# Optimization experiments

Hardware: AMD Instinct MI355X
Metric: run time of the kernel (lower is better)

The kernel has to match this reference:

```python
import jax, jax.numpy as jnp
import numpy as np

B, C, H, W = 8, 256, 64, 64
HEADS, HID = 8, 64
TMP = HEADS * HID  # 512


def setup_inputs() -> dict:
    key = jax.random.key(0)
    ks = jax.random.split(key, 6)
    s = lambda fan: 1.0 / np.sqrt(fan)
    fmap = jax.random.normal(ks[0], (B, C, H, W), jnp.float32)
    Wq = jax.random.normal(ks[1], (TMP, C), jnp.float32) * s(C)          # to_q 1x1 conv (no bias)
    Wdw = jax.random.normal(ks[2], (C, 1, 3, 3), jnp.float32) * s(9)     # depthwise 3x3 (groups=C, no bias)
    Wkv = jax.random.normal(ks[3], (2 * TMP, C), jnp.float32) * s(C)     # 1x1 conv producing k,v (no bias)
    Wout = jax.random.normal(ks[4], (C, TMP), jnp.float32) * s(TMP)      # to_out 1x1 conv
    bout = jax.random.normal(ks[5], (C,), jnp.float32) * 0.01
    return {"fmap": fmap, "Wq": Wq, "Wdw": Wdw, "Wkv": Wkv, "Wout": Wout, "bout": bout}


def reference(fmap, Wq, Wdw, Wkv, Wout, bout):
    heads, hid = HEADS, HID
    scale = hid ** (-0.5)
    b, c, h, w = fmap.shape
    n = h * w

    # 1x1 conv == channel GEMM
    q = jnp.einsum('bcxy,oc->boxy', fmap, Wq)
    # depthwise 3x3, padding=1
    dw = jax.lax.conv_general_dilated(
        fmap, Wdw, window_strides=(1, 1), padding='SAME',
        dimension_numbers=('NCHW', 'OIHW', 'NCHW'), feature_group_count=c)
    kv = jnp.einsum('bcxy,oc->boxy', dw, Wkv)
    k, v = jnp.split(kv, 2, axis=1)

    # 'b (h c) x y -> b h (x y) c'
    def to_seq(t):
        return t.reshape(b, heads, hid, n).transpose(0, 1, 3, 2)  # [b, h, n, d]

    q, k, v = to_seq(q), to_seq(k), to_seq(v)
    q = jax.nn.softmax(q, axis=-1) * scale   # softmax over feature dim
    k = jax.nn.softmax(k, axis=-2)           # softmax over token dim

    ctx = jnp.einsum('bhnd,bhne->bhde', k, v)    # [b, h, d, d]
    out = jnp.einsum('bhnd,bhde->bhne', q, ctx)  # [b, h, n, d]

    # '(b h) (x y) d -> b (h d) x y'
    out = out.transpose(0, 1, 3, 2).reshape(b, heads * hid, h, w)

    # to_out: GELU (exact) then 1x1 conv with bias (mode='ac')
    out = jax.nn.gelu(out, approximate=False)
    return jnp.einsum('bcxy,oc->boxy', out, Wout) + bout[None, :, None, None]
```

## Files before the change

kernel.cpp:

```cpp
#include <hip/hip_runtime.h>
#include <hip/hip_bf16.h>
#include <math.h>

#define Bx 8
#define Cc 256
#define Nn 4096
#define TMPc 512

typedef unsigned short ushort;
typedef unsigned int uint;
typedef unsigned long long ull;
typedef __attribute__((ext_vector_type(8))) short bf16x8;
typedef __attribute__((ext_vector_type(4))) float f32x4;

union F4 { float4 v; float f[4]; };

__device__ __forceinline__ ushort f2bf(float x) {
  uint u = __float_as_uint(x);
  uint r = (u + 0x7fffu + ((u >> 16) & 1u)) >> 16;
  return (ushort)r;
}
__device__ __forceinline__ float gelu_fast(float x) {
  float u = 0.70710678118654752f * x;
  float au = fabsf(u);
  float t = __builtin_amdgcn_rcpf(1.0f + 0.3275911f * au);
  float poly = ((((1.061405429f * t - 1.453152027f) * t + 1.421413741f) * t -
                 0.284496736f) * t + 0.254829592f) * t;
  float e = 1.0f - poly * __expf(-u * u);
  float erfu = copysignf(e, u);
  return 0.5f * x * (1.0f + erfu);
}

typedef const __attribute__((address_space(1))) uint* gp1_t;
typedef __attribute__((address_space(3))) uint* lp3_t;
__device__ __forceinline__ void gload16(void* lds, const void* g) {
  __builtin_amdgcn_global_load_lds((gp1_t)g, (lp3_t)lds, 16, 0, 0);
}
__device__ __forceinline__ void lgkm_fence() {
  asm volatile("s_waitcnt lgkmcnt(0)" ::: "memory");
}
__device__ __forceinline__ bf16x8 fragread(const char* lds, int row, int kc) {
  return *(const bf16x8*)(lds + row * 64 + ((kc ^ (row & 3)) << 4));
}
__device__ __forceinline__ void stage2(char* buf, const ushort* src, int ld,
                                       int row0, int col, int w, int prow, int gst) {
  int off = __builtin_amdgcn_readfirstlane(w * 2048);
  gload16(buf + off, src + (size_t)(row0 + prow) * ld + col + gst * 8);
  gload16(buf + off + 1024, src + (size_t)(row0 + 16 + prow) * ld + col + gst * 8);
}

#define CGRP 32
__global__ __launch_bounds__(256) void convfuse_k(const float* __restrict__ fmap,
                                                  const float* __restrict__ Wdw,
                                                  ushort* __restrict__ fmapT,
                                                  ushort* __restrict__ dwT) {
  __shared__ float sin_[CGRP][6 * 64 + 1];
  __shared__ float wl[CGRP][9];
  int t = threadIdx.x;
  int y0 = blockIdx.x * 4;
  int c0 = blockIdx.y * CGRP;
  int z = blockIdx.z;
  for (int i = t; i < CGRP * 9; i += 256) wl[i / 9][i % 9] = Wdw[c0 * 9 + i];
  const float* src = fmap + ((size_t)z * Cc + c0) * 4096;
#pragma unroll
  for (int it = 0; it < 12; ++it) {
    int idx = it * 256 + t;
    int c = idx / 96, rem = idx % 96, yy = rem >> 4, x4 = rem & 15;
    int gy = y0 - 1 + yy;
    F4 v;
    if ((unsigned)gy < 64u)
      v.v = *(const float4*)&src[(size_t)c * 4096 + gy * 64 + x4 * 4];
    else
      v.f[0] = v.f[1] = v.f[2] = v.f[3] = 0.f;
#pragma unroll
    for (int j = 0; j < 4; ++j) sin_[c][yy * 64 + x4 * 4 + j] = v.f[j];
  }
  __syncthreads();
  int c8 = (t & 3) * 8;
  int nl = t >> 2;
  size_t nbase = (size_t)z * 4096 + (size_t)y0 * 64;
#pragma unroll
  for (int it = 0; it < 4; ++it) {
    int n = it * 64 + nl;
    int y = n >> 6, x = n & 63;
    union { ushort u[8]; uint4 q; } fo, go;
#pragma unroll
    for (int cc = 0; cc < 8; ++cc) {
      int c = c8 + cc;
      fo.u[cc] = f2bf(sin_[c][(y + 1) * 64 + x]);
      float acc = 0.f;
#pragma unroll
      for (int dy = 0; dy < 3; ++dy) {
#pragma unroll
        for (int dx = 0; dx < 3; ++dx) {
          int xx = x + dx - 1;
          float pv = ((unsigned)xx < 64u) ? sin_[c][(y + dy) * 64 + xx] : 0.f;
          acc += pv * wl[c][dy * 3 + dx];
        }
      }
      go.u[cc] = f2bf(acc);
    }
    *(uint4*)&fmapT[(nbase + n) * Cc + c0 + c8] = fo.q;
    *(uint4*)&dwT[(nbase + n) * Cc + c0 + c8] = go.q;
  }
}

__global__ __launch_bounds__(256) void cvtb3_k(const float* __restrict__ Wq,
                                               const float* __restrict__ Wkv,
                                               const float* __restrict__ Wout,
                                               ushort* __restrict__ WqB,
                                               ushort* __restrict__ WkvB,
                                               ushort* __restrict__ WoutB) {
  int i = blockIdx.x * 256 + threadIdx.x;
  const float* s;
  ushort* d;
  int idx;
  if (i < 32768) { s = Wq; d = WqB; idx = i; }
  else if (i < 98304) { s = Wkv; d = WkvB; idx = i - 32768; }
  else { s = Wout; d = WoutB; idx = i - 98304; }
  F4 v; v.v = *(const float4*)&s[(size_t)idx * 4];
  union { ushort u[4]; uint2 q; } o;
#pragma unroll
  for (int j = 0; j < 4; ++j) o.u[j] = f2bf(v.f[j]);
  *(uint2*)&d[(size_t)idx * 4] = o.q;
}

__global__ __launch_bounds__(256, 2) void kvgemm3_k(const ushort* __restrict__ WkvB,
                                                    const ushort* __restrict__ dwT,
                                                    ushort* __restrict__ kv) {
  __shared__ __align__(16) char lds[57344];
  char* Bres = lds;
  char* Asg  = lds + 32768;
  int t = threadIdx.x, w = t >> 6, l = t & 63;
  int z = blockIdx.y, n0 = blockIdx.x * 64;
  int rl = l & 15, kc = l >> 4;
  int prow = l >> 2;
  int gst = (l & 3) ^ ((l >> 2) & 3);

  const ushort* dT = dwT + ((size_t)z * 4096 + n0) * 256;
#pragma unroll
  for (int p = 0; p < 8; ++p) {
    int row = (w * 8 + p) * 2 + (l >> 5);
    int cs = l & 31;
    int off = __builtin_amdgcn_readfirstlane((w * 8 + p) * 1024);
    gload16(Bres + off, dT + (size_t)row * 256 + ((cs ^ (row & 7)) * 8));
  }
  stage2(Asg, WkvB, 256, w * 32, 0, w, prow, gst);
  stage2(Asg + 8192, WkvB, 256, w * 32, 32, w, prow, gst);
  asm volatile("s_waitcnt vmcnt(0)" ::: "memory");
  __syncthreads();

  ushort* kz = kv + (size_t)z * 1024 * 4096;
#pragma unroll
  for (int c = 0; c < 8; ++c) {
    f32x4 acc[2][4];
#pragma unroll
    for (int i = 0; i < 2; ++i)
#pragma unroll
      for (int j = 0; j < 4; ++j) acc[i][j] = (f32x4){0.f, 0.f, 0.f, 0.f};
#pragma unroll
    for (int k0 = 0; k0 < 8; ++k0) {
      int s = c * 8 + k0;
      if (s + 2 < 64) {
        int s2 = s + 2;
        lgkm_fence();
        stage2(Asg + (s2 % 3) * 8192, WkvB, 256, (s2 >> 3) * 128 + w * 32,
               (s2 & 7) * 32, w, prow, gst);
      }
      if (s < 62) asm volatile("s_waitcnt vmcnt(4)" ::: "memory");
      else if (s == 62) asm volatile("s_waitcnt vmcnt(2)" ::: "memory");
      else asm volatile("s_waitcnt vmcnt(0)" ::: "memory");
      const char* bp = Asg + (s % 3) * 8192 + w * 2048;
      bf16x8 a0 = fragread(bp, rl, kc);
      bf16x8 a1 = fragread(bp, 16 + rl, kc);
#pragma unroll
      for (int j = 0; j < 4; ++j) {
        int n = 16 * j + rl;
        bf16x8 b = *(const bf16x8*)(Bres + n * 512 + (((k0 * 4 + kc) ^ (n & 7)) << 4));
        acc[0][j] = __builtin_amdgcn_mfma_f32_16x16x32_bf16(a0, b, acc[0][j], 0, 0, 0);
        acc[1][j] = __builtin_amdgcn_mfma_f32_16x16x32_bf16(a1, b, acc[1][j], 0, 0, 0);
      }
    }
#pragma unroll
    for (int i = 0; i < 2; ++i) {
#pragma unroll
      for (int reg = 0; reg < 4; ++reg) {
        int r = c * 128 + w * 32 + 16 * i + 4 * kc + reg;
#pragma unroll
        for (int j = 0; j < 4; ++j) {
          int col = n0 + 16 * j + rl;
          float v = acc[i][j][reg];
          kz[(size_t)r * 4096 + col] = f2bf(c < 4 ? __expf(v) : v);
        }
      }
    }
  }
}

__global__ __launch_bounds__(256) void ctx_mfma(const ushort* __restrict__ kv,
                                                float* __restrict__ ctxf,
                                                float* __restrict__ sf) {
  __shared__ __align__(16) char lds[16384];
  int t = threadIdx.x, w = t >> 6, l = t & 63;
  int s = blockIdx.x;
  int h = blockIdx.y & 7, z = blockIdx.y >> 3;
  const ushort* kb = kv + ((size_t)z * 1024 + h * 64) * 4096;
  const ushort* vb = kv + ((size_t)z * 1024 + 512 + h * 64) * 4096;
  f32x4 acc[2][2];
  f32x4 accs[2];
#pragma unroll
  for (int i = 0; i < 2; ++i) {
    accs[i] = (f32x4){0.f, 0.f, 0.f, 0.f};
#pragma unroll
    for (int j = 0; j < 2; ++j) acc[i][j] = (f32x4){0.f, 0.f, 0.f, 0.f};
  }
  bf16x8 ones;
#pragma unroll
  for (int i = 0; i < 8; ++i) ones[i] = (short)0x3F80;
  int wr = (w >> 1) * 32, wc = (w & 1) * 32;
  int rl = l & 15, kc = l >> 4;
  int srow = (l >> 2) & 15, scol = l & 3;
  int row = w * 16 + srow;
  int g = scol ^ (row & 3);
  int soff = __builtin_amdgcn_readfirstlane(w * 1024);
#define CSTG(bb, it)                                                      \
  {                                                                       \
    int k0_ = s * 512 + (it) * 32;                                        \
    gload16(lds + (bb) + soff, vb + (size_t)row * 4096 + k0_ + g * 8);    \
    gload16(lds + (bb) + 4096 + soff, kb + (size_t)row * 4096 + k0_ + g * 8); \
  }
  CSTG(0, 0);
  asm volatile("s_waitcnt vmcnt(0)" ::: "memory");
  __syncthreads();
  for (int it = 0; it < 16; ++it) {
    int cur = (it & 1) << 13;
    if (it + 1 < 16) CSTG(cur ^ 8192, it + 1);
    bf16x8 a[2], b[2];
#pragma unroll
    for (int i = 0; i < 2; ++i) a[i] = fragread(lds + cur, wr + i * 16 + rl, kc);
#pragma unroll
    for (int i = 0; i < 2; ++i) b[i] = fragread(lds + cur + 4096, wc + i * 16 + rl, kc);
#pragma unroll
    for (int i = 0; i < 2; ++i)
#pragma unroll
      for (int j = 0; j < 2; ++j)
        acc[i][j] = __builtin_amdgcn_mfma_f32_16x16x32_bf16(a[i], b[j], acc[i][j], 0, 0, 0);
    if (w < 2) {
#pragma unroll
      for (int j = 0; j < 2; ++j)
        accs[j] = __builtin_amdgcn_mfma_f32_16x16x32_bf16(b[j], ones, accs[j], 0, 0, 0);
    }
    asm volatile("s_waitcnt vmcnt(0)" ::: "memory");
    __syncthreads();
  }
  float* cf = ctxf + (size_t)(z * 8 + h) * 4096;
#pragma unroll
  for (int i = 0; i < 2; ++i)
#pragma unroll
    for (int reg = 0; reg < 4; ++reg) {
      int e = wr + i * 16 + kc * 4 + reg;
#pragma unroll
      for (int j = 0; j < 2; ++j) {
        int d = wc + j * 16 + rl;
        atomicAdd(&cf[e * 64 + d], acc[i][j][reg]);
      }
    }
  if (w < 2 && rl == 0) {
    float* sp = sf + (size_t)(z * 8 + h) * 64;
#pragma unroll
    for (int j = 0; j < 2; ++j)
#pragma unroll
      for (int reg = 0; reg < 4; ++reg)
        atomicAdd(&sp[wc + j * 16 + kc * 4 + reg], accs[j][reg]);
  }
#undef CSTG
}

__global__ __launch_bounds__(256) void ctx_cvt(const float* __restrict__ ctxf,
                                               const float* __restrict__ sf,
                                               ushort* __restrict__ ctxb) {
  int page = blockIdx.x;
  const float* s = ctxf + (size_t)page * 4096;
  const float* sp = sf + (size_t)page * 64;
  ushort* d = ctxb + (size_t)page * 4096;
  int t = threadIdx.x;
  int e = t >> 2, d0 = (t & 3) * 16;
  union { ushort u[16]; uint4 q[2]; } o;
#pragma unroll
  for (int j = 0; j < 16; ++j) {
    int dd = d0 + j;
    o.u[j] = f2bf(s[e * 64 + dd] / sp[dd]);
  }
  uint4* dp = (uint4*)&d[e * 64 + d0];
  dp[0] = o.q[0]; dp[1] = o.q[1];
}

__global__ __launch_bounds__(256, 2) void qao_k(const ushort* __restrict__ fmapT,
                                                const ushort* __restrict__ WqB,
                                                const ushort* __restrict__ ctxb,
                                                const ushort* __restrict__ WoutB,
                                                const float* __restrict__ bout,
                                                float* __restrict__ out) {
  __shared__ __align__(16) char lds[73728];
  __shared__ float wsum[4][64];
  char* qbuf = lds;
  char* Bres = lds + 16384;
  char* Asg  = lds + 49152;
  int t = threadIdx.x, w = t >> 6, l = t & 63;
  int z = blockIdx.y, n0 = blockIdx.x * 64;
  int rl = l & 15, kc = l >> 4;
  int prow = l >> 2;
  int gst = (l & 3) ^ ((l >> 2) & 3);
  int hh = w >> 1;
  int wcn = (w & 1) * 32;

  const ushort* fT = fmapT + ((size_t)z * 4096 + n0) * 256;
#pragma unroll
  for (int p = 0; p < 8; ++p) {
    int row = (w * 8 + p) * 2 + (l >> 5);
    int cs = l & 31;
    int off = __builtin_amdgcn_readfirstlane((w * 8 + p) * 1024);
    gload16(Bres + off, fT + (size_t)row * 256 + ((cs ^ (row & 7)) * 8));
  }
  stage2(Asg, WqB, 256, w * 32, 0, w, prow, gst);
  stage2(Asg + 8192, WqB, 256, w * 32, 32, w, prow, gst);

  f32x4 oacc[4][4];
#pragma unroll
  for (int i = 0; i < 4; ++i)
#pragma unroll
    for (int j = 0; j < 4; ++j) oacc[i][j] = (f32x4){0.f, 0.f, 0.f, 0.f};

  asm volatile("s_waitcnt vmcnt(0)" ::: "memory");
  __syncthreads();

  for (int c = 0; c < 4; ++c) {
    const ushort* Wqc = WqB + (size_t)(c * 128) * 256;
    f32x4 qa[2][4];
#pragma unroll
    for (int i = 0; i < 2; ++i)
#pragma unroll
      for (int j = 0; j < 4; ++j) qa[i][j] = (f32x4){0.f, 0.f, 0.f, 0.f};
#pragma unroll
    for (int k0 = 0; k0 < 8; ++k0) {
      if (k0 + 2 < 8) {
        lgkm_fence();
        stage2(Asg + ((k0 + 2) % 3) * 8192, Wqc, 256, w * 32, (k0 + 2) * 32, w, prow, gst);
      }
      if (k0 < 6) asm volatile("s_waitcnt vmcnt(4)" ::: "memory");
      else if (k0 == 6) asm volatile("s_waitcnt vmcnt(2)" ::: "memory");
      else asm volatile("s_waitcnt vmcnt(0)" ::: "memory");
      const char* bp = Asg + (k0 % 3) * 8192 + w * 2048;
      bf16x8 a0 = fragread(bp, rl, kc);
      bf16x8 a1 = fragread(bp, 16 + rl, kc);
#pragma unroll
      for (int j = 0; j < 4; ++j) {
        int n = 16 * j + rl;
        bf16x8 b = *(const bf16x8*)(Bres + n * 512 + (((k0 * 4 + kc) ^ (n & 7)) << 4));
        qa[0][j] = __builtin_amdgcn_mfma_f32_16x16x32_bf16(a0, b, qa[0][j], 0, 0, 0);
        qa[1][j] = __builtin_amdgcn_mfma_f32_16x16x32_bf16(a1, b, qa[1][j], 0, 0, 0);
      }
    }
    const ushort* cpg = ctxb + (size_t)(z * 8 + c * 2 + hh) * 4096;
    bf16x8 ca[2][4];
#pragma unroll
    for (int s2 = 0; s2 < 2; ++s2)
#pragma unroll
      for (int i = 0; i < 4; ++i)
        ca[s2][i] = *(const bf16x8*)(cpg + (size_t)(16 * i + rl) * 64 + s2 * 32 + kc * 8);
    float sj[4];
#pragma unroll
    for (int j = 0; j < 4; ++j) {
      float s = 0.f;
#pragma unroll
      for (int i = 0; i < 2; ++i)
#pragma unroll
        for (int reg = 0; reg < 4; ++reg) {
          float e = __expf(qa[i][j][reg]);
          qa[i][j][reg] = e;
          s += e;
        }
      s += __shfl_xor(s, 16, 64);
      s += __shfl_xor(s, 32, 64);
      sj[j] = s;
    }
    if (l < 16) {
#pragma unroll
      for (int j = 0; j < 4; ++j) wsum[w][j * 16 + l] = sj[j];
    }
    __syncthreads();
#pragma unroll
    for (int j = 0; j < 4; ++j) {
      float tot = wsum[w][16 * j + rl] + wsum[w ^ 1][16 * j + rl];
      float inv = 0.125f / tot;
#pragma unroll
      for (int i = 0; i < 2; ++i)
#pragma unroll
        for (int reg = 0; reg < 4; ++reg) qa[i][j][reg] *= inv;
    }
#pragma unroll
    for (int i = 0; i < 2; ++i)
#pragma unroll
      for (int j = 0; j < 4; ++j) {
        int n = 16 * j + rl;
        int dby = (w * 32 + 16 * i + 4 * kc) * 2;
        union { ushort u[4]; ull q; } pk;
#pragma unroll
        for (int reg = 0; reg < 4; ++reg) pk.u[reg] = f2bf(qa[i][j][reg]);
        *(ull*)(qbuf + n * 256 + (dby ^ ((n & 7) << 4))) = pk.q;
      }
    __syncthreads();
    f32x4 pacc[4][2];
#pragma unroll
    for (int i = 0; i < 4; ++i)
#pragma unroll
      for (int j = 0; j < 2; ++j) pacc[i][j] = (f32x4){0.f, 0.f, 0.f, 0.f};
#pragma unroll
    for (int s2 = 0; s2 < 2; ++s2) {
      bf16x8 pb[2];
#pragma unroll
      for (int j = 0; j < 2; ++j) {
        int n = wcn + 16 * j + rl;
        int dby = hh * 128 + s2 * 64 + kc * 16;
        pb[j] = *(const bf16x8*)(qbuf + n * 256 + (dby ^ ((n & 7) << 4)));
      }
#pragma unroll
      for (int i = 0; i < 4; ++i)
#pragma unroll
        for (int j = 0; j < 2; ++j)
          pacc[i][j] = __builtin_amdgcn_mfma_f32_16x16x32_bf16(ca[s2][i], pb[j], pacc[i][j], 0, 0, 0);
    }
#pragma unroll
    for (int i = 0; i < 4; ++i)
#pragma unroll
      for (int j = 0; j < 2; ++j) {
        int n = wcn + 16 * j + rl;
        int mby = (hh * 64 + 16 * i + 4 * kc) * 2;
        union { ushort u[4]; ull q; } pk;
#pragma unroll
        for (int reg = 0; reg < 4; ++reg) pk.u[reg] = f2bf(gelu_fast(pacc[i][j][reg]));
        *(ull*)(qbuf + n * 256 + (mby ^ ((n & 7) << 4))) = pk.q;
      }
    __syncthreads();
    stage2(Asg, WoutB, 512, w * 64, c * 128, w, prow, gst);
    stage2(Asg + 8192, WoutB, 512, w * 64 + 32, c * 128, w, prow, gst);
    bf16x8 ob[4];
#pragma unroll
    for (int s = 0; s < 8; ++s) {
      if (s + 2 < 8) {
        int s2 = s + 2;
        lgkm_fence();
        stage2(Asg + (s2 % 3) * 8192, WoutB, 512, w * 64 + (s2 & 1) * 32,
               c * 128 + (s2 >> 1) * 32, w, prow, gst);
      }
      if (s < 6) asm volatile("s_waitcnt vmcnt(4)" ::: "memory");
      else if (s == 6) asm volatile("s_waitcnt vmcnt(2)" ::: "memory");
      else asm volatile("s_waitcnt vmcnt(0)" ::: "memory");
      int half = s & 1, ks = s >> 1;
      if (half == 0) {
#pragma unroll
        for (int j = 0; j < 4; ++j) {
          int n = 16 * j + rl;
          ob[j] = *(const bf16x8*)(qbuf + n * 256 + ((ks * 64 + kc * 16) ^ ((n & 7) << 4)));
        }
      }
      const char* bp = Asg + (s % 3) * 8192 + w * 2048;
      bf16x8 a0 = fragread(bp, rl, kc);
      bf16x8 a1 = fragread(bp, 16 + rl, kc);
#pragma unroll
      for (int j = 0; j < 4; ++j) {
        oacc[half * 2][j] = __builtin_amdgcn_mfma_f32_16x16x32_bf16(a0, ob[j], oacc[half * 2][j], 0, 0, 0);
        oacc[half * 2 + 1][j] = __builtin_amdgcn_mfma_f32_16x16x32_bf16(a1, ob[j], oacc[half * 2 + 1][j], 0, 0, 0);
      }
    }
    if (c < 3) {
      const ushort* Wqn = WqB + (size_t)((c + 1) * 128) * 256;
      lgkm_fence();
      stage2(Asg, Wqn, 256, w * 32, 0, w, prow, gst);
      stage2(Asg + 8192, Wqn, 256, w * 32, 32, w, prow, gst);
    }
  }
  float* oz = out + (size_t)z * Cc * Nn + n0;
#pragma unroll
  for (int i = 0; i < 4; ++i) {
#pragma unroll
    for (int reg = 0; reg < 4; ++reg) {
      int crow = w * 64 + 16 * i + 4 * kc + reg;
      float bv = bout[crow];
      float* rowp = oz + (size_t)crow * 4096;
#pragma unroll
      for (int j = 0; j < 4; ++j) rowp[16 * j + rl] = oacc[i][j][reg] + bv;
    }
  }
}

extern "C" void kernel_launch(void* const* d_in, const int* in_sizes, int n_in,
                              void* d_out, int out_size, void* d_ws, size_t ws_size,
                              hipStream_t stream) {
  (void)in_sizes; (void)n_in; (void)out_size; (void)ws_size;
  const float* fmap = (const float*)d_in[0];
  const float* Wq   = (const float*)d_in[1];
  const float* Wdw  = (const float*)d_in[2];
  const float* Wkv  = (const float*)d_in[3];
  const float* Wout = (const float*)d_in[4];
  const float* bout = (const float*)d_in[5];
  float* out = (float*)d_out;

  ushort* WqB   = (ushort*)d_ws;
  ushort* WkvB  = WqB + 512 * 256;
  ushort* WoutB = WkvB + 1024 * 256;
  ushort* fmapT = WoutB + 256 * 512;
  ushort* dwT   = fmapT + (size_t)Bx * 4096 * 256;
  ushort* kv    = dwT + (size_t)Bx * 4096 * 256;
  ushort* ctxb  = kv + (size_t)Bx * 1024 * 4096;
  float*  ctxf  = (float*)(ctxb + (size_t)Bx * 8 * 4096);
  float*  sf    = ctxf + (size_t)Bx * 8 * 64 * 64;

  hipMemsetAsync(ctxf, 0, (size_t)Bx * 8 * (4096 + 64) * sizeof(float), stream);
  cvtb3_k<<<dim3(512), 256, 0, stream>>>(Wq, Wkv, Wout, WqB, WkvB, WoutB);
  convfuse_k<<<dim3(16, Cc / CGRP, Bx), 256, 0, stream>>>(fmap, Wdw, fmapT, dwT);
  kvgemm3_k<<<dim3(64, Bx), 256, 0, stream>>>(WkvB, dwT, kv);
  ctx_mfma<<<dim3(8, Bx * 8), 256, 0, stream>>>(kv, ctxf, sf);
  ctx_cvt<<<dim3(Bx * 8), 256, 0, stream>>>(ctxf, sf, ctxb);
  qao_k<<<dim3(64, Bx), 256, 0, stream>>>(fmapT, WqB, ctxb, WoutB, bout, out);
}
```

Before: 121.4 us.

## Fuse weight conversion into conv kernel, reuse conv rows in registers, raise MFMA priority

Folds the weight bf16 conversion kernel into the depthwise conv kernel as an extra z-slice of blocks, removing one kernel launch. The conv inner loop now has each thread own one column across four output rows, loading six input rows per channel into registers and reusing them for the 3x3 stencil instead of re-reading LDS for every tap. MFMA loops in the GEMM kernels are wrapped with s_setprio so waves issuing matrix ops get scheduling priority. This raises register pressure in the conv kernel, and the priority hints may not help with few waves per SIMD.

```diff
diff --git a/kernel.cpp b/kernel.cpp
--- a/kernel.cpp
+++ b/kernel.cpp
@@ -50,13 +50,38 @@
 }
 
 #define CGRP 32
-__global__ __launch_bounds__(256) void convfuse_k(const float* __restrict__ fmap,
-                                                  const float* __restrict__ Wdw,
-                                                  ushort* __restrict__ fmapT,
-                                                  ushort* __restrict__ dwT) {
+__global__ __launch_bounds__(256) void convw_k(const float* __restrict__ fmap,
+                                               const float* __restrict__ Wdw,
+                                               ushort* __restrict__ fmapT,
+                                               ushort* __restrict__ dwT,
+                                               const float* __restrict__ Wq,
+                                               const float* __restrict__ Wkv,
+                                               const float* __restrict__ Wout,
+                                               ushort* __restrict__ WqB,
+                                               ushort* __restrict__ WkvB,
+                                               ushort* __restrict__ WoutB) {
   __shared__ float sin_[CGRP][6 * 64 + 1];
   __shared__ float wl[CGRP][9];
   int t = threadIdx.x;
+  if (blockIdx.z == 8) {
+    int wid = blockIdx.y * 16 + blockIdx.x;
+#pragma unroll
+    for (int g = 0; g < 4; ++g) {
+      int i = wid * 1024 + g * 256 + t;
+      const float* s;
+      ushort* d;
+      int idx;
+      if (i < 32768) { s = Wq; d = WqB; idx = i; }
+      else if (i < 98304) { s = Wkv; d = WkvB; idx = i - 32768; }
+      else { s = Wout; d = WoutB; idx = i - 98304; }
+      F4 v; v.v = *(const float4*)&s[(size_t)idx * 4];
+      union { ushort u[4]; uint2 q; } o;
+#pragma unroll
+      for (int j = 0; j < 4; ++j) o.u[j] = f2bf(v.f[j]);
+      *(uint2*)&d[(size_t)idx * 4] = o.q;
+    }
+    return;
+  }
   int y0 = blockIdx.x * 4;
   int c0 = blockIdx.y * CGRP;
   int z = blockIdx.z;
@@ -77,52 +102,39 @@
   }
   __syncthreads();
   int c8 = (t & 3) * 8;
-  int nl = t >> 2;
+  int x = t >> 2;
   size_t nbase = (size_t)z * 4096 + (size_t)y0 * 64;
+  union { ushort u[8]; uint4 q; } fo[4], go[4];
+#pragma unroll
+  for (int cc = 0; cc < 8; ++cc) {
+    int c = c8 + cc;
+    float wr[9];
+#pragma unroll
+    for (int k = 0; k < 9; ++k) wr[k] = wl[c][k];
+    float r[6][3];
+#pragma unroll
+    for (int row = 0; row < 6; ++row) {
+      r[row][1] = sin_[c][row * 64 + x];
+      r[row][0] = (x > 0) ? sin_[c][row * 64 + x - 1] : 0.f;
+      r[row][2] = (x < 63) ? sin_[c][row * 64 + x + 1] : 0.f;
+    }
+#pragma unroll
+    for (int it = 0; it < 4; ++it) {
+      fo[it].u[cc] = f2bf(r[it + 1][1]);
+      float acc = 0.f;
+#pragma unroll
+      for (int dy = 0; dy < 3; ++dy)
+#pragma unroll
+        for (int dx = 0; dx < 3; ++dx)
+          acc += r[it + dy][dx] * wr[dy * 3 + dx];
+      go[it].u[cc] = f2bf(acc);
+    }
+  }
 #pragma unroll
   for (int it = 0; it < 4; ++it) {
-    int n = it * 64 + nl;
-    int y = n >> 6, x = n & 63;
-    union { ushort u[8]; uint4 q; } fo, go;
-#pragma unroll
-    for (int cc = 0; cc < 8; ++cc) {
-      int c = c8 + cc;
-      fo.u[cc] = f2bf(sin_[c][(y + 1) * 64 + x]);
-      float acc = 0.f;
-#pragma unroll
-      for (int dy = 0; dy < 3; ++dy) {
-#pragma unroll
-        for (int dx = 0; dx < 3; ++dx) {
-          int xx = x + dx - 1;
-          float pv = ((unsigned)xx < 64u) ? sin_[c][(y + dy) * 64 + xx] : 0.f;
-          acc += pv * wl[c][dy * 3 + dx];
-        }
-      }
-      go.u[cc] = f2bf(acc);
-    }
-    *(uint4*)&fmapT[(nbase + n) * Cc + c0 + c8] = fo.q;
-    *(uint4*)&dwT[(nbase + n) * Cc + c0 + c8] = go.q;
-  }
-}
-
-__global__ __launch_bounds__(256) void cvtb3_k(const float* __restrict__ Wq,
-                                               const float* __restrict__ Wkv,
-                                               const float* __restrict__ Wout,
-                                               ushort* __restrict__ WqB,
-                                               ushort* __restrict__ WkvB,
-                                               ushort* __restrict__ WoutB) {
-  int i = blockIdx.x * 256 + threadIdx.x;
-  const float* s;
-  ushort* d;
-  int idx;
-  if (i < 32768) { s = Wq; d = WqB; idx = i; }
-  else if (i < 98304) { s = Wkv; d = WkvB; idx = i - 32768; }
-  else { s = Wout; d = WoutB; idx = i - 98304; }
-  F4 v; v.v = *(const float4*)&s[(size_t)idx * 4];
-  union { ushort u[4]; uint2 q; } o;
-#pragma unroll
-  for (int j = 0; j < 4; ++j) o.u[j] = f2bf(v.f[j]);
-  *(uint2*)&d[(size_t)idx * 4] = o.q;
+    *(uint4*)&fmapT[(nbase + it * 64 + x) * Cc + c0 + c8] = fo[it].q;
+    *(uint4*)&dwT[(nbase + it * 64 + x) * Cc + c0 + c8] = go[it].q;
+  }
 }
 
 __global__ __launch_bounds__(256, 2) void kvgemm3_k(const ushort* __restrict__ WkvB,
@@ -173,6 +185,7 @@
       const char* bp = Asg + (s % 3) * 8192 + w * 2048;
       bf16x8 a0 = fragread(bp, rl, kc);
       bf16x8 a1 = fragread(bp, 16 + rl, kc);
+      __builtin_amdgcn_s_setprio(1);
 #pragma unroll
       for (int j = 0; j < 4; ++j) {
         int n = 16 * j + rl;
@@ -180,6 +193,7 @@
         acc[0][j] = __builtin_amdgcn_mfma_f32_16x16x32_bf16(a0, b, acc[0][j], 0, 0, 0);
         acc[1][j] = __builtin_amdgcn_mfma_f32_16x16x32_bf16(a1, b, acc[1][j], 0, 0, 0);
       }
+      __builtin_amdgcn_s_setprio(0);
     }
 #pragma unroll
     for (int i = 0; i < 2; ++i) {
@@ -353,6 +367,7 @@
       const char* bp = Asg + (k0 % 3) * 8192 + w * 2048;
       bf16x8 a0 = fragread(bp, rl, kc);
       bf16x8 a1 = fragread(bp, 16 + rl, kc);
+      __builtin_amdgcn_s_setprio(1);
 #pragma unroll
       for (int j = 0; j < 4; ++j) {
         int n = 16 * j + rl;
@@ -360,6 +375,7 @@
         qa[0][j] = __builtin_amdgcn_mfma_f32_16x16x32_bf16(a0, b, qa[0][j], 0, 0, 0);
         qa[1][j] = __builtin_amdgcn_mfma_f32_16x16x32_bf16(a1, b, qa[1][j], 0, 0, 0);
       }
+      __builtin_amdgcn_s_setprio(0);
     }
     const ushort* cpg = ctxb + (size_t)(z * 8 + c * 2 + hh) * 4096;
     bf16x8 ca[2][4];
@@ -415,6 +431,7 @@
     for (int i = 0; i < 4; ++i)
 #pragma unroll
       for (int j = 0; j < 2; ++j) pacc[i][j] = (f32x4){0.f, 0.f, 0.f, 0.f};
+    __builtin_amdgcn_s_setprio(1);
 #pragma unroll
     for (int s2 = 0; s2 < 2; ++s2) {
       bf16x8 pb[2];
@@ -430,6 +447,7 @@
         for (int j = 0; j < 2; ++j)
           pacc[i][j] = __builtin_amdgcn_mfma_f32_16x16x32_bf16(ca[s2][i], pb[j], pacc[i][j], 0, 0, 0);
     }
+    __builtin_amdgcn_s_setprio(0);
 #pragma unroll
     for (int i = 0; i < 4; ++i)
 #pragma unroll
@@ -467,11 +485,13 @@
       const char* bp = Asg + (s % 3) * 8192 + w * 2048;
       bf16x8 a0 = fragread(bp, rl, kc);
       bf16x8 a1 = fragread(bp, 16 + rl, kc);
+      __builtin_amdgcn_s_setprio(1);
 #pragma unroll
       for (int j = 0; j < 4; ++j) {
         oacc[half * 2][j] = __builtin_amdgcn_mfma_f32_16x16x32_bf16(a0, ob[j], oacc[half * 2][j], 0, 0, 0);
         oacc[half * 2 + 1][j] = __builtin_amdgcn_mfma_f32_16x16x32_bf16(a1, ob[j], oacc[half * 2 + 1][j], 0, 0, 0);
       }
+      __builtin_amdgcn_s_setprio(0);
     }
     if (c < 3) {
       const ushort* Wqn = WqB + (size_t)((c + 1) * 128) * 256;
@@ -517,8 +537,8 @@
   float*  sf    = ctxf + (size_t)Bx * 8 * 64 * 64;
 
   hipMemsetAsync(ctxf, 0, (size_t)Bx * 8 * (4096 + 64) * sizeof(float), stream);
-  cvtb3_k<<<dim3(512), 256, 0, stream>>>(Wq, Wkv, Wout, WqB, WkvB, WoutB);
-  convfuse_k<<<dim3(16, Cc / CGRP, Bx), 256, 0, stream>>>(fmap, Wdw, fmapT, dwT);
+  convw_k<<<dim3(16, 8, 9), 256, 0, stream>>>(fmap, Wdw, fmapT, dwT,
+                                              Wq, Wkv, Wout, WqB, WkvB, WoutB);
   kvgemm3_k<<<dim3(64, Bx), 256, 0, stream>>>(WkvB, dwT, kv);
   ctx_mfma<<<dim3(8, Bx * 8), 256, 0, stream>>>(kv, ctxf, sf);
   ctx_cvt<<<dim3(Bx * 8), 256, 0, stream>>>(ctxf, sf, ctxb);
```

Result: faster. 118.9 us (-2.1%).
